# Kernel tuning notes

Hardware: AMD Instinct MI355X
Metric: run time of the kernel (lower is better)

The kernel has to match this reference:

```python
import jax, jax.numpy as jnp
import numpy as np

B, R, H, W = 8, 128, 4096, 4096

def setup_inputs() -> dict:
    key = jax.random.key(0)
    k1, k2, k3, k4 = jax.random.split(key, 4)
    N = jax.random.normal(k1, (B, 1, R, W), dtype=jnp.float32)
    Ak_L = jax.random.normal(k2, (B, 1, H, W), dtype=jnp.float32)
    alpha = jax.random.uniform(k3, (B,), dtype=jnp.float32)
    gamma = jax.random.uniform(k4, (B,), dtype=jnp.float32)
    return {"N": N, "Ak_L": Ak_L, "alpha": alpha, "gamma": gamma}

def reference(N, Ak_L, alpha, gamma):
    # N: [B,1,r,W], Ak_L: [B,1,H,W], alpha/gamma: [B]
    b = N.shape[0]
    r = N.shape[2]
    a = alpha.reshape(b, 1, 1, 1)
    g = gamma.reshape(b, 1, 1, 1)
    I = jnp.eye(r, dtype=N.dtype)  # broadcast over [B,1,r,r]
    # C = alpha*I + 2*gamma * N @ N^T  -> [B,1,r,r]
    C = a * I + 2.0 * g * jnp.einsum('bcrw,bcsw->bcrs', N, N)
    Cinv = jnp.linalg.pinv(C)  # batched pinv over [B,1]
    # X = (Ak_L @ N^T) @ pinv(C) -> [B,1,H,r]
    AN = jnp.einsum('bchw,bcrw->bchr', Ak_L, N)
    X = jnp.einsum('bchr,bcrs->bchs', AN, Cinv)
    return 2.0 * g * X
```

## Files before the change

### kernel.cpp

```cpp
#include <hip/hip_runtime.h>


typedef __attribute__((ext_vector_type(8))) short bf16x8;
typedef __attribute__((ext_vector_type(4))) float f32x4;
typedef __attribute__((ext_vector_type(4))) unsigned int u32x4;

#define MFMA16(a, b, c) __builtin_amdgcn_mfma_f32_16x16x32_bf16((a), (b), (c), 0, 0, 0)
#define NSPLIT 8

__device__ __forceinline__ unsigned short f2bf(float f) {
  union { float f; unsigned u; } v; v.f = f;
  unsigned u = v.u;
  return (unsigned short)((u + 0x7FFFu + ((u >> 16) & 1u)) >> 16);
}
__device__ __forceinline__ unsigned pack2(float x, float y) {
  return (unsigned)f2bf(x) | ((unsigned)f2bf(y) << 16);
}

__global__ __launch_bounds__(256) void k_castT(const float* __restrict__ N,
                                               unsigned short* __restrict__ NT) {
  __attribute__((aligned(16))) __shared__ float tile[128 * 68];
  int wc = blockIdx.x, b = blockIdx.y;
  const float* Nb = N + (size_t)b * 524288 + wc * 64;
  int t = threadIdx.x;
  int row = t >> 1, half = t & 1;
  const float* src = Nb + (size_t)row * 4096 + half * 32;
  float* dst = tile + row * 68 + half * 32;
#pragma unroll
  for (int j = 0; j < 8; j++) *(f32x4*)(dst + j * 4) = *(const f32x4*)(src + j * 4);
  __syncthreads();
  int ow = t >> 2, q = t & 3;
  unsigned short* out = NT + (size_t)b * 524288 + (size_t)(wc * 64 + ow) * 128 + q * 32;
#pragma unroll
  for (int c = 0; c < 4; c++) {
    u32x4 p;
#pragma unroll
    for (int k = 0; k < 4; k++) {
      float f0 = tile[(q * 32 + c * 8 + k * 2) * 68 + ow];
      float f1 = tile[(q * 32 + c * 8 + k * 2 + 1) * 68 + ow];
      p[k] = pack2(f0, f1);
    }
    *(u32x4*)(out + c * 8) = p;
  }
}

__global__ __launch_bounds__(256) void k_gram(const float* __restrict__ N,
                                              float* __restrict__ Gpart) {
  __attribute__((aligned(16))) __shared__ unsigned short lds[128 * 72];
  int ks = blockIdx.x, b = blockIdx.y;
  const float* Nb = N + (size_t)b * 524288 + ks * 512;
  int t = threadIdx.x;
  int wave = t >> 6, lane = t & 63, quad = lane >> 4, l16 = lane & 15;
  f32x4 acc[2][8];
#pragma unroll
  for (int i = 0; i < 2; i++)
#pragma unroll
    for (int j = 0; j < 8; j++) acc[i][j] = (f32x4){0.f, 0.f, 0.f, 0.f};
  int srow = t >> 1, shalf = t & 1;
  const float* srcb = Nb + (size_t)srow * 4096 + shalf * 32;
  unsigned short* dptr = lds + srow * 72 + shalf * 32;
  for (int it = 0; it < 8; ++it) {
    u32x4 pk0, pk1;
    {
      f32x4 v0 = *(const f32x4*)(srcb + it * 64 + 0);
      f32x4 v1 = *(const f32x4*)(srcb + it * 64 + 4);
      f32x4 v2 = *(const f32x4*)(srcb + it * 64 + 8);
      f32x4 v3 = *(const f32x4*)(srcb + it * 64 + 12);
      pk0[0] = pack2(v0[0], v0[1]); pk0[1] = pack2(v0[2], v0[3]);
      pk0[2] = pack2(v1[0], v1[1]); pk0[3] = pack2(v1[2], v1[3]);
      pk1[0] = pack2(v2[0], v2[1]); pk1[1] = pack2(v2[2], v2[3]);
      pk1[2] = pack2(v3[0], v3[1]); pk1[3] = pack2(v3[2], v3[3]);
    }
    u32x4 pk2, pk3;
    {
      f32x4 v0 = *(const f32x4*)(srcb + it * 64 + 16);
      f32x4 v1 = *(const f32x4*)(srcb + it * 64 + 20);
      f32x4 v2 = *(const f32x4*)(srcb + it * 64 + 24);
      f32x4 v3 = *(const f32x4*)(srcb + it * 64 + 28);
      pk2[0] = pack2(v0[0], v0[1]); pk2[1] = pack2(v0[2], v0[3]);
      pk2[2] = pack2(v1[0], v1[1]); pk2[3] = pack2(v1[2], v1[3]);
      pk3[0] = pack2(v2[0], v2[1]); pk3[1] = pack2(v2[2], v2[3]);
      pk3[2] = pack2(v3[0], v3[1]); pk3[3] = pack2(v3[2], v3[3]);
    }
    __syncthreads();
    *(u32x4*)(dptr + 0) = pk0;
    *(u32x4*)(dptr + 8) = pk1;
    *(u32x4*)(dptr + 16) = pk2;
    *(u32x4*)(dptr + 24) = pk3;
    __syncthreads();
    bf16x8 af[2][2], bfv[8][2];
#pragma unroll
    for (int mt = 0; mt < 2; mt++)
#pragma unroll
      for (int kk = 0; kk < 2; kk++)
        af[mt][kk] = *(const bf16x8*)(lds + (wave * 32 + mt * 16 + l16) * 72 + (kk * 4 + quad) * 8);
#pragma unroll
    for (int nt = 0; nt < 8; nt++)
#pragma unroll
      for (int kk = 0; kk < 2; kk++)
        bfv[nt][kk] = *(const bf16x8*)(lds + (nt * 16 + l16) * 72 + (kk * 4 + quad) * 8);
#pragma unroll
    for (int mt = 0; mt < 2; mt++)
#pragma unroll
      for (int nt = 0; nt < 8; nt++)
#pragma unroll
        for (int kk = 0; kk < 2; kk++)
          acc[mt][nt] = MFMA16(af[mt][kk], bfv[nt][kk], acc[mt][nt]);
  }
  float* Gp = Gpart + ((size_t)(b * NSPLIT + ks) << 14);
#pragma unroll
  for (int mt = 0; mt < 2; mt++)
#pragma unroll
    for (int nt = 0; nt < 8; nt++)
#pragma unroll
      for (int rg = 0; rg < 4; rg++) {
        int row = wave * 32 + mt * 16 + quad * 4 + rg;
        int col = nt * 16 + l16;
        Gp[row * 128 + col] = acc[mt][nt][rg];
      }
}

__global__ __launch_bounds__(1024) void k_inv(const float* __restrict__ Gpart,
                                              const float* __restrict__ alpha,
                                              const float* __restrict__ gamma,
                                              float* __restrict__ Cinv) {
  __attribute__((aligned(16))) __shared__ float Cs[16384];
  __attribute__((aligned(16))) __shared__ float mcol[2][128];
  __attribute__((aligned(16))) __shared__ float pivrow[2][128];
  int b = blockIdx.x;
  int t = threadIdx.x;
  const float* Gp = Gpart + ((size_t)b * NSPLIT << 14);
#pragma unroll
  for (int c = 0; c < 4; c++) {
    int off = c * 4096 + t * 4;
    f32x4 s = (f32x4){0.f, 0.f, 0.f, 0.f};
#pragma unroll
    for (int ks = 0; ks < NSPLIT; ks++) s += *(const f32x4*)(Gp + ks * 16384 + off);
    *(f32x4*)(Cs + off) = s;
  }
  __syncthreads();
  int cg = t & 31, rb = t >> 5;
  float al = alpha[b], ga2 = 2.f * gamma[b];
  float a[4][4];
#pragma unroll
  for (int i = 0; i < 4; i++) {
    int r = rb * 4 + i;
    f32x4 v = *(const f32x4*)(Cs + r * 128 + cg * 4);
#pragma unroll
    for (int j = 0; j < 4; j++) {
      int c = cg * 4 + j;
      a[i][j] = ga2 * v[j] + ((r == c) ? al : 0.f);
    }
  }
  for (int p = 0; p < 128; ++p) {
    int pb = p & 1;
    int cgp = p >> 2, jp = p & 3;
    int rbp = p >> 2, ip = p & 3;
    if (cg == cgp) {
      f32x4 mv;
#pragma unroll
      for (int i = 0; i < 4; i++)
        mv[i] = (jp & 2) ? ((jp & 1) ? a[i][3] : a[i][2]) : ((jp & 1) ? a[i][1] : a[i][0]);
      *(f32x4*)&mcol[pb][rb * 4] = mv;
    }
    if (rb == rbp) {
      f32x4 pv;
#pragma unroll
      for (int j = 0; j < 4; j++)
        pv[j] = (ip & 2) ? ((ip & 1) ? a[3][j] : a[2][j]) : ((ip & 1) ? a[1][j] : a[0][j]);
      *(f32x4*)&pivrow[pb][cg * 4] = pv;
    }
    __syncthreads();
    float invd = 1.0f / mcol[pb][p];
    f32x4 mc = *(const f32x4*)&mcol[pb][rb * 4];
    f32x4 pr = *(const f32x4*)&pivrow[pb][cg * 4];
#pragma unroll
    for (int i = 0; i < 4; i++) {
      int r = rb * 4 + i;
      float mi = mc[i] * invd;
#pragma unroll
      for (int j = 0; j < 4; j++) {
        int c = cg * 4 + j;
        float v = a[i][j] - mi * pr[j];
        if (c == p) v = -mi;
        if (r == p) v = pr[j] * invd;
        if (r == p && c == p) v = invd;
        a[i][j] = v;
      }
    }
  }
  float* dst = Cinv + ((size_t)b << 14);
#pragma unroll
  for (int i = 0; i < 4; i++) {
    int r = rb * 4 + i;
    *(f32x4*)(dst + r * 128 + cg * 4) = (f32x4){a[i][0], a[i][1], a[i][2], a[i][3]};
  }
}

__global__ __launch_bounds__(256) void k_mt(const float* __restrict__ Cinv,
                                            const unsigned short* __restrict__ NT,
                                            const float* __restrict__ gamma,
                                            unsigned short* __restrict__ Mt) {
  __attribute__((aligned(16))) __shared__ unsigned short la[128 * 72];
  __attribute__((aligned(16))) __shared__ unsigned short lb[128 * 72];
  int wc = blockIdx.x, b = blockIdx.y;
  int w0 = wc * 128;
  float ga2 = 2.f * gamma[b];
  const float* Cb = Cinv + ((size_t)b << 14);
  const unsigned short* NTb = NT + (size_t)b * 524288;
  int t = threadIdx.x, wave = t >> 6, lane = t & 63, quad = lane >> 4, l16 = lane & 15;
  f32x4 acc[2][8];
#pragma unroll
  for (int i = 0; i < 2; i++)
#pragma unroll
    for (int j = 0; j < 8; j++) acc[i][j] = (f32x4){0.f, 0.f, 0.f, 0.f};
  int row = t >> 1, half = t & 1;
  const float* asrc = Cb + (size_t)row * 128 + half * 32;
  const unsigned short* bsrc = NTb + (size_t)(w0 + row) * 128 + half * 32;
  unsigned short* adst = la + row * 72 + half * 32;
  unsigned short* bdst = lb + row * 72 + half * 32;
  for (int it = 0; it < 2; ++it) {
    int k0 = it * 64;
    u32x4 pa0, pa1;
    {
      f32x4 v0 = *(const f32x4*)(asrc + k0 + 0);
      f32x4 v1 = *(const f32x4*)(asrc + k0 + 4);
      f32x4 v2 = *(const f32x4*)(asrc + k0 + 8);
      f32x4 v3 = *(const f32x4*)(asrc + k0 + 12);
      pa0[0] = pack2(ga2 * v0[0], ga2 * v0[1]); pa0[1] = pack2(ga2 * v0[2], ga2 * v0[3]);
      pa0[2] = pack2(ga2 * v1[0], ga2 * v1[1]); pa0[3] = pack2(ga2 * v1[2], ga2 * v1[3]);
      pa1[0] = pack2(ga2 * v2[0], ga2 * v2[1]); pa1[1] = pack2(ga2 * v2[2], ga2 * v2[3]);
      pa1[2] = pack2(ga2 * v3[0], ga2 * v3[1]); pa1[3] = pack2(ga2 * v3[2], ga2 * v3[3]);
    }
    u32x4 pa2, pa3;
    {
      f32x4 v0 = *(const f32x4*)(asrc + k0 + 16);
      f32x4 v1 = *(const f32x4*)(asrc + k0 + 20);
      f32x4 v2 = *(const f32x4*)(asrc + k0 + 24);
      f32x4 v3 = *(const f32x4*)(asrc + k0 + 28);
      pa2[0] = pack2(ga2 * v0[0], ga2 * v0[1]); pa2[1] = pack2(ga2 * v0[2], ga2 * v0[3]);
      pa2[2] = pack2(ga2 * v1[0], ga2 * v1[1]); pa2[3] = pack2(ga2 * v1[2], ga2 * v1[3]);
      pa3[0] = pack2(ga2 * v2[0], ga2 * v2[1]); pa3[1] = pack2(ga2 * v2[2], ga2 * v2[3]);
      pa3[2] = pack2(ga2 * v3[0], ga2 * v3[1]); pa3[3] = pack2(ga2 * v3[2], ga2 * v3[3]);
    }
    u32x4 bv0 = *(const u32x4*)(bsrc + k0 + 0);
    u32x4 bv1 = *(const u32x4*)(bsrc + k0 + 8);
    u32x4 bv2 = *(const u32x4*)(bsrc + k0 + 16);
    u32x4 bv3 = *(const u32x4*)(bsrc + k0 + 24);
    __syncthreads();
    *(u32x4*)(adst + 0) = pa0;  *(u32x4*)(adst + 8) = pa1;
    *(u32x4*)(adst + 16) = pa2; *(u32x4*)(adst + 24) = pa3;
    *(u32x4*)(bdst + 0) = bv0;  *(u32x4*)(bdst + 8) = bv1;
    *(u32x4*)(bdst + 16) = bv2; *(u32x4*)(bdst + 24) = bv3;
    __syncthreads();
    bf16x8 af[2][2], bfv[8][2];
#pragma unroll
    for (int mt = 0; mt < 2; mt++)
#pragma unroll
      for (int kk = 0; kk < 2; kk++)
        af[mt][kk] = *(const bf16x8*)(la + (wave * 32 + mt * 16 + l16) * 72 + (kk * 4 + quad) * 8);
#pragma unroll
    for (int nt = 0; nt < 8; nt++)
#pragma unroll
      for (int kk = 0; kk < 2; kk++)
        bfv[nt][kk] = *(const bf16x8*)(lb + (nt * 16 + l16) * 72 + (kk * 4 + quad) * 8);
#pragma unroll
    for (int mt = 0; mt < 2; mt++)
#pragma unroll
      for (int nt = 0; nt < 8; nt++)
#pragma unroll
        for (int kk = 0; kk < 2; kk++)
          acc[mt][nt] = MFMA16(af[mt][kk], bfv[nt][kk], acc[mt][nt]);
    __syncthreads();
  }
  unsigned short* Mb = Mt + (size_t)b * 524288;
#pragma unroll
  for (int mt = 0; mt < 2; mt++)
#pragma unroll
    for (int nt = 0; nt < 8; nt++)
#pragma unroll
      for (int rg = 0; rg < 4; rg++) {
        int r = wave * 32 + mt * 16 + quad * 4 + rg;
        int w = w0 + nt * 16 + l16;
        Mb[(size_t)r * 4096 + w] = f2bf(acc[mt][nt][rg]);
      }
}

__global__ __launch_bounds__(256) void k_gemm(const float* __restrict__ A,
                                              const unsigned short* __restrict__ Mt,
                                              float* __restrict__ out) {
  __attribute__((aligned(16))) __shared__ unsigned short la[64 * 72];
  __attribute__((aligned(16))) __shared__ unsigned short lb[128 * 72];
  int blk = blockIdx.x;
  int b = blk & 7, mtile = blk >> 3;
  const float* Ab = A + (size_t)b * 16777216 + (size_t)mtile * 64 * 4096;
  const unsigned short* Mb = Mt + (size_t)b * 524288;
  int t = threadIdx.x, wave = t >> 6, lane = t & 63, quad = lane >> 4, l16 = lane & 15;
  int wm = wave >> 1, wr = wave & 1;
  f32x4 acc[2][4];
#pragma unroll
  for (int i = 0; i < 2; i++)
#pragma unroll
    for (int j = 0; j < 4; j++) acc[i][j] = (f32x4){0.f, 0.f, 0.f, 0.f};
  int arow = t >> 2, aq = t & 3;
  int brow = t >> 1, bhalf = t & 1;
  const float* asrc = Ab + (size_t)arow * 4096 + aq * 16;
  const unsigned short* bsrc = Mb + (size_t)brow * 4096 + bhalf * 32;
  unsigned short* adst = la + arow * 72 + aq * 16;
  unsigned short* bdst = lb + brow * 72 + bhalf * 32;
  f32x4 av0 = *(const f32x4*)(asrc + 0);
  f32x4 av1 = *(const f32x4*)(asrc + 4);
  f32x4 av2 = *(const f32x4*)(asrc + 8);
  f32x4 av3 = *(const f32x4*)(asrc + 12);
  u32x4 bv0 = *(const u32x4*)(bsrc + 0);
  u32x4 bv1 = *(const u32x4*)(bsrc + 8);
  u32x4 bv2 = *(const u32x4*)(bsrc + 16);
  u32x4 bv3 = *(const u32x4*)(bsrc + 24);
  for (int it = 0; it < 64; ++it) {
    u32x4 pa0, pa1;
    pa0[0] = pack2(av0[0], av0[1]); pa0[1] = pack2(av0[2], av0[3]);
    pa0[2] = pack2(av1[0], av1[1]); pa0[3] = pack2(av1[2], av1[3]);
    pa1[0] = pack2(av2[0], av2[1]); pa1[1] = pack2(av2[2], av2[3]);
    pa1[2] = pack2(av3[0], av3[1]); pa1[3] = pack2(av3[2], av3[3]);
    __syncthreads();
    *(u32x4*)(adst + 0) = pa0;
    *(u32x4*)(adst + 8) = pa1;
    *(u32x4*)(bdst + 0) = bv0;
    *(u32x4*)(bdst + 8) = bv1;
    *(u32x4*)(bdst + 16) = bv2;
    *(u32x4*)(bdst + 24) = bv3;
    __syncthreads();
    if (it < 63) {
      int k0 = (it + 1) * 64;
      av0 = *(const f32x4*)(asrc + k0 + 0);
      av1 = *(const f32x4*)(asrc + k0 + 4);
      av2 = *(const f32x4*)(asrc + k0 + 8);
      av3 = *(const f32x4*)(asrc + k0 + 12);
      bv0 = *(const u32x4*)(bsrc + k0 + 0);
      bv1 = *(const u32x4*)(bsrc + k0 + 8);
      bv2 = *(const u32x4*)(bsrc + k0 + 16);
      bv3 = *(const u32x4*)(bsrc + k0 + 24);
    }
    bf16x8 af[2][2], bfv[4][2];
#pragma unroll
    for (int mt = 0; mt < 2; mt++)
#pragma unroll
      for (int kk = 0; kk < 2; kk++)
        af[mt][kk] = *(const bf16x8*)(la + (wm * 32 + mt * 16 + l16) * 72 + (kk * 4 + quad) * 8);
#pragma unroll
    for (int rt = 0; rt < 4; rt++)
#pragma unroll
      for (int kk = 0; kk < 2; kk++)
        bfv[rt][kk] = *(const bf16x8*)(lb + (wr * 64 + rt * 16 + l16) * 72 + (kk * 4 + quad) * 8);
#pragma unroll
    for (int mt = 0; mt < 2; mt++)
#pragma unroll
      for (int rt = 0; rt < 4; rt++)
#pragma unroll
        for (int kk = 0; kk < 2; kk++)
          acc[mt][rt] = MFMA16(af[mt][kk], bfv[rt][kk], acc[mt][rt]);
  }
  float* ob = out + (size_t)b * 524288 + (size_t)mtile * 64 * 128;
#pragma unroll
  for (int mt = 0; mt < 2; mt++)
#pragma unroll
    for (int rt = 0; rt < 4; rt++)
#pragma unroll
      for (int rg = 0; rg < 4; rg++) {
        int h = wm * 32 + mt * 16 + quad * 4 + rg;
        int r = wr * 64 + rt * 16 + l16;
        ob[h * 128 + r] = acc[mt][rt][rg];
      }
}

extern "C" void kernel_launch(void* const* d_in, const int* in_sizes, int n_in,
                              void* d_out, int out_size, void* d_ws, size_t ws_size,
                              hipStream_t stream) {
  const float* N = (const float*)d_in[0];
  const float* Ak = (const float*)d_in[1];
  const float* alpha = (const float*)d_in[2];
  const float* gamma = (const float*)d_in[3];
  float* out = (float*)d_out;
  char* ws = (char*)d_ws;
  unsigned short* NT = (unsigned short*)(ws);
  float* Gpart = (float*)(ws + 8388608);
  float* Cinv = (float*)(ws + 12582912);
  unsigned short* Mt = (unsigned short*)(ws + 13107200);

  k_castT<<<dim3(64, 8), 256, 0, stream>>>(N, NT);
  k_gram<<<dim3(NSPLIT, 8), 256, 0, stream>>>(N, Gpart);
  k_inv<<<dim3(8), 1024, 0, stream>>>(Gpart, alpha, gamma, Cinv);
  k_mt<<<dim3(32, 8), 256, 0, stream>>>(Cinv, NT, gamma, Mt);
  k_gemm<<<dim3(512), 256, 0, stream>>>(Ak, Mt, out);
}
```

Baseline: 861.7 us.

## Double-buffer LDS in k_gemm with two-deep register prefetch and one barrier per step

The main GEMM kernel now uses two LDS buffers and two register sets of prefetched global data, alternating between them. This lets each k-step get by with a single barrier instead of two, and gives global loads two iterations of latency hiding. The cost is double the LDS and more live registers, which may lower occupancy. A sched_barrier pins instruction ordering. Reuse of a buffer two steps later relies on the intervening barrier for WAR safety.

```diff
diff --git a/kernel.cpp b/kernel.cpp
--- a/kernel.cpp
+++ b/kernel.cpp
@@ -286,11 +286,63 @@
       }
 }
 
+__device__ __forceinline__ void gemm_step(
+    f32x4& A0, f32x4& A1, f32x4& A2, f32x4& A3,
+    u32x4& B0, u32x4& B1, u32x4& B2, u32x4& B3,
+    unsigned short* adst, unsigned short* bdst,
+    const unsigned short* lap, const unsigned short* lbp,
+    const float* asrc, const unsigned short* bsrc,
+    int next_k0, int do_pf, int wm, int wr, int quad, int l16,
+    f32x4 (&acc)[2][4]) {
+  u32x4 pa0, pa1;
+  pa0[0] = pack2(A0[0], A0[1]); pa0[1] = pack2(A0[2], A0[3]);
+  pa0[2] = pack2(A1[0], A1[1]); pa0[3] = pack2(A1[2], A1[3]);
+  pa1[0] = pack2(A2[0], A2[1]); pa1[1] = pack2(A2[2], A2[3]);
+  pa1[2] = pack2(A3[0], A3[1]); pa1[3] = pack2(A3[2], A3[3]);
+  *(u32x4*)(adst + 0) = pa0;
+  *(u32x4*)(adst + 8) = pa1;
+  *(u32x4*)(bdst + 0) = B0;
+  *(u32x4*)(bdst + 8) = B1;
+  *(u32x4*)(bdst + 16) = B2;
+  *(u32x4*)(bdst + 24) = B3;
+  asm volatile("s_waitcnt lgkmcnt(0)" ::: "memory");
+  __builtin_amdgcn_s_barrier();
+  __builtin_amdgcn_sched_barrier(0);
+  if (do_pf) {
+    A0 = *(const f32x4*)(asrc + next_k0 + 0);
+    A1 = *(const f32x4*)(asrc + next_k0 + 4);
+    A2 = *(const f32x4*)(asrc + next_k0 + 8);
+    A3 = *(const f32x4*)(asrc + next_k0 + 12);
+    B0 = *(const u32x4*)(bsrc + next_k0 + 0);
+    B1 = *(const u32x4*)(bsrc + next_k0 + 8);
+    B2 = *(const u32x4*)(bsrc + next_k0 + 16);
+    B3 = *(const u32x4*)(bsrc + next_k0 + 24);
+  }
+  bf16x8 af[2][2], bfv[4][2];
+#pragma unroll
+  for (int mt = 0; mt < 2; mt++)
+#pragma unroll
+    for (int kk = 0; kk < 2; kk++)
+      af[mt][kk] = *(const bf16x8*)(lap + (wm * 32 + mt * 16 + l16) * 72 + (kk * 4 + quad) * 8);
+#pragma unroll
+  for (int rt = 0; rt < 4; rt++)
+#pragma unroll
+    for (int kk = 0; kk < 2; kk++)
+      bfv[rt][kk] = *(const bf16x8*)(lbp + (wr * 64 + rt * 16 + l16) * 72 + (kk * 4 + quad) * 8);
+#pragma unroll
+  for (int mt = 0; mt < 2; mt++)
+#pragma unroll
+    for (int rt = 0; rt < 4; rt++)
+#pragma unroll
+      for (int kk = 0; kk < 2; kk++)
+        acc[mt][rt] = MFMA16(af[mt][kk], bfv[rt][kk], acc[mt][rt]);
+}
+
 __global__ __launch_bounds__(256) void k_gemm(const float* __restrict__ A,
                                               const unsigned short* __restrict__ Mt,
                                               float* __restrict__ out) {
-  __attribute__((aligned(16))) __shared__ unsigned short la[64 * 72];
-  __attribute__((aligned(16))) __shared__ unsigned short lb[128 * 72];
+  __attribute__((aligned(16))) __shared__ unsigned short la[2][64 * 72];
+  __attribute__((aligned(16))) __shared__ unsigned short lb[2][128 * 72];
   int blk = blockIdx.x;
   int b = blk & 7, mtile = blk >> 3;
   const float* Ab = A + (size_t)b * 16777216 + (size_t)mtile * 64 * 4096;
@@ -306,59 +358,34 @@
   int brow = t >> 1, bhalf = t & 1;
   const float* asrc = Ab + (size_t)arow * 4096 + aq * 16;
   const unsigned short* bsrc = Mb + (size_t)brow * 4096 + bhalf * 32;
-  unsigned short* adst = la + arow * 72 + aq * 16;
-  unsigned short* bdst = lb + brow * 72 + bhalf * 32;
-  f32x4 av0 = *(const f32x4*)(asrc + 0);
-  f32x4 av1 = *(const f32x4*)(asrc + 4);
-  f32x4 av2 = *(const f32x4*)(asrc + 8);
-  f32x4 av3 = *(const f32x4*)(asrc + 12);
-  u32x4 bv0 = *(const u32x4*)(bsrc + 0);
-  u32x4 bv1 = *(const u32x4*)(bsrc + 8);
-  u32x4 bv2 = *(const u32x4*)(bsrc + 16);
-  u32x4 bv3 = *(const u32x4*)(bsrc + 24);
-  for (int it = 0; it < 64; ++it) {
-    u32x4 pa0, pa1;
-    pa0[0] = pack2(av0[0], av0[1]); pa0[1] = pack2(av0[2], av0[3]);
-    pa0[2] = pack2(av1[0], av1[1]); pa0[3] = pack2(av1[2], av1[3]);
-    pa1[0] = pack2(av2[0], av2[1]); pa1[1] = pack2(av2[2], av2[3]);
-    pa1[2] = pack2(av3[0], av3[1]); pa1[3] = pack2(av3[2], av3[3]);
-    __syncthreads();
-    *(u32x4*)(adst + 0) = pa0;
-    *(u32x4*)(adst + 8) = pa1;
-    *(u32x4*)(bdst + 0) = bv0;
-    *(u32x4*)(bdst + 8) = bv1;
-    *(u32x4*)(bdst + 16) = bv2;
-    *(u32x4*)(bdst + 24) = bv3;
-    __syncthreads();
-    if (it < 63) {
-      int k0 = (it + 1) * 64;
-      av0 = *(const f32x4*)(asrc + k0 + 0);
-      av1 = *(const f32x4*)(asrc + k0 + 4);
-      av2 = *(const f32x4*)(asrc + k0 + 8);
-      av3 = *(const f32x4*)(asrc + k0 + 12);
-      bv0 = *(const u32x4*)(bsrc + k0 + 0);
-      bv1 = *(const u32x4*)(bsrc + k0 + 8);
-      bv2 = *(const u32x4*)(bsrc + k0 + 16);
-      bv3 = *(const u32x4*)(bsrc + k0 + 24);
-    }
-    bf16x8 af[2][2], bfv[4][2];
-#pragma unroll
-    for (int mt = 0; mt < 2; mt++)
-#pragma unroll
-      for (int kk = 0; kk < 2; kk++)
-        af[mt][kk] = *(const bf16x8*)(la + (wm * 32 + mt * 16 + l16) * 72 + (kk * 4 + quad) * 8);
-#pragma unroll
-    for (int rt = 0; rt < 4; rt++)
-#pragma unroll
-      for (int kk = 0; kk < 2; kk++)
-        bfv[rt][kk] = *(const bf16x8*)(lb + (wr * 64 + rt * 16 + l16) * 72 + (kk * 4 + quad) * 8);
-#pragma unroll
-    for (int mt = 0; mt < 2; mt++)
-#pragma unroll
-      for (int rt = 0; rt < 4; rt++)
-#pragma unroll
-        for (int kk = 0; kk < 2; kk++)
-          acc[mt][rt] = MFMA16(af[mt][kk], bfv[rt][kk], acc[mt][rt]);
+  unsigned short* adst0 = &la[0][arow * 72 + aq * 16];
+  unsigned short* adst1 = &la[1][arow * 72 + aq * 16];
+  unsigned short* bdst0 = &lb[0][brow * 72 + bhalf * 32];
+  unsigned short* bdst1 = &lb[1][brow * 72 + bhalf * 32];
+  f32x4 xa0 = *(const f32x4*)(asrc + 0);
+  f32x4 xa1 = *(const f32x4*)(asrc + 4);
+  f32x4 xa2 = *(const f32x4*)(asrc + 8);
+  f32x4 xa3 = *(const f32x4*)(asrc + 12);
+  u32x4 xb0 = *(const u32x4*)(bsrc + 0);
+  u32x4 xb1 = *(const u32x4*)(bsrc + 8);
+  u32x4 xb2 = *(const u32x4*)(bsrc + 16);
+  u32x4 xb3 = *(const u32x4*)(bsrc + 24);
+  f32x4 ya0 = *(const f32x4*)(asrc + 64);
+  f32x4 ya1 = *(const f32x4*)(asrc + 68);
+  f32x4 ya2 = *(const f32x4*)(asrc + 72);
+  f32x4 ya3 = *(const f32x4*)(asrc + 76);
+  u32x4 yb0 = *(const u32x4*)(bsrc + 64);
+  u32x4 yb1 = *(const u32x4*)(bsrc + 72);
+  u32x4 yb2 = *(const u32x4*)(bsrc + 80);
+  u32x4 yb3 = *(const u32x4*)(bsrc + 88);
+  for (int itp = 0; itp < 32; ++itp) {
+    int pf = (itp < 31);
+    gemm_step(xa0, xa1, xa2, xa3, xb0, xb1, xb2, xb3,
+              adst0, bdst0, &la[0][0], &lb[0][0], asrc, bsrc,
+              (2 * itp + 2) * 64, pf, wm, wr, quad, l16, acc);
+    gemm_step(ya0, ya1, ya2, ya3, yb0, yb1, yb2, yb3,
+              adst1, bdst1, &la[1][0], &lb[1][0], asrc, bsrc,
+              (2 * itp + 3) * 64, pf, wm, wr, quad, l16, acc);
   }
   float* ob = out + (size_t)b * 524288 + (size_t)mtile * 64 * 128;
 #pragma unroll
```

Result: no change. 854.5 us (-0.8%).
